# Performance work log

Hardware: AMD Instinct MI355X
Metric: run time of the kernel (lower is better)

## Reference

```python
import jax, jax.numpy as jnp
import numpy as np

L, D, H, B, SX, SY, VS, VT = 6, 1024, 16, 4, 512, 512, 32000, 32000
DK = D // H
FF = 4 * D
EPS = 1e-3          # LayerNorm eps (added to std, not var)
SCALE_EMB = float(np.sqrt(D))
NEG = -1e30         # stands in for -inf; fully-masked rows are zeroed after softmax


def pos_encoding(length, d):
    # tensor2tensor-style sinusoid: [sin | cos] concatenated along channels
    nt = d // 2
    lti = np.log(1e4) / (nt - 1)
    inv = np.exp(np.arange(nt) * -lti)
    st = np.arange(length)[:, None] * inv[None, :]
    return jnp.asarray(np.concatenate([np.sin(st), np.cos(st)], axis=1), jnp.float32)


def layer_norm(z, a, b):
    # faithful to the torch module: uses unbiased std (ddof=1) and divides by (std + eps)
    mu = z.mean(-1, keepdims=True)
    sig = jnp.sqrt(((z - mu) ** 2).sum(-1, keepdims=True) / (z.shape[-1] - 1))
    return (z - mu) / (sig + EPS) * a + b


def mha(xq, xkv, wq, wk, wv, wo, mask):
    # xq: (b, lq, D), xkv: (b, lk, D); head-chunking of channel dim == reshape to (H, DK)
    b, lq, _ = xq.shape
    q = (xq @ wq.T).reshape(b, lq, H, DK)
    k = (xkv @ wk.T).reshape(b, -1, H, DK)
    v = (xkv @ wv.T).reshape(b, -1, H, DK)
    s = jnp.einsum('bqhd,bkhd->bhqk', q, k) * (1.0 / np.sqrt(DK))
    m = mask[:, None, :, :]
    s = jnp.where(m, s, NEG)
    att = jax.nn.softmax(s, axis=-1)
    att = att * m.any(-1, keepdims=True)  # replicates NaN->0 for fully masked rows
    c = jnp.einsum('bhqk,bkhd->bqhd', att, v).reshape(b, lq, D)
    return c @ wo.T


def setup_inputs():
    key = jax.random.key(0)
    ks = jax.random.split(key, 10)
    s = 0.02
    emb_x = (jax.random.normal(ks[0], (VS, D), jnp.float32) * s).at[0].set(0.0)  # padding_idx=0
    emb_y = (jax.random.normal(ks[1], (VT, D), jnp.float32) * s).at[0].set(0.0)
    return {
        'emb_x': emb_x, 'emb_y': emb_y,
        'enc_qkvo': jax.random.normal(ks[2], (L, 4, D, D), jnp.float32) * s,
        'enc_ln_s': jnp.ones((L, 2, D), jnp.float32), 'enc_ln_b': jnp.zeros((L, 2, D), jnp.float32),
        'enc_w1': jax.random.normal(ks[3], (L, FF, D), jnp.float32) * s, 'enc_b1': jnp.zeros((L, FF), jnp.float32),
        'enc_w2': jax.random.normal(ks[4], (L, D, FF), jnp.float32) * s, 'enc_b2': jnp.zeros((L, D), jnp.float32),
        'dec_qkvo': jax.random.normal(ks[5], (L, 8, D, D), jnp.float32) * s,
        'dec_ln_s': jnp.ones((L, 3, D), jnp.float32), 'dec_ln_b': jnp.zeros((L, 3, D), jnp.float32),
        'dec_w1': jax.random.normal(ks[6], (L, FF, D), jnp.float32) * s, 'dec_b1': jnp.zeros((L, FF), jnp.float32),
        'dec_w2': jax.random.normal(ks[7], (L, D, FF), jnp.float32) * s, 'dec_b2': jnp.zeros((L, D), jnp.float32),
        'x_block': jax.random.randint(ks[8], (B, SX), 0, VS),
        'y_block': jax.random.randint(ks[9], (B, SY), 0, VT),
    }


def reference(emb_x, emb_y, enc_qkvo, enc_ln_s, enc_ln_b, enc_w1, enc_b1, enc_w2, enc_b2,
              dec_qkvo, dec_ln_s, dec_ln_b, dec_w1, dec_b1, dec_w2, dec_b2, x_block, y_block):
    # internal layout (b, len, D); torch code uses (b, D, len) -- math is identical
    ex = emb_x[x_block] * SCALE_EMB + pos_encoding(SX, D)[None]
    ey = emb_y[y_block] * SCALE_EMB + pos_encoding(SY, D)[None]
    xv = x_block != 0
    yv = y_block != 0
    xx = xv[:, :, None] & xv[:, None, :]                                   # (B, qx, kx)
    xy = yv[:, :, None] & xv[:, None, :]                                   # (B, qy, kx)
    yy = (yv[:, :, None] & yv[:, None, :]) & jnp.tril(jnp.ones((SY, SY), bool))[None]
    e = ex
    for i in range(L):
        sub = mha(e, e, enc_qkvo[i, 0], enc_qkvo[i, 1], enc_qkvo[i, 2], enc_qkvo[i, 3], xx)
        e = layer_norm(e + sub, enc_ln_s[i, 0], enc_ln_b[i, 0])
        sub = jax.nn.relu(e @ enc_w1[i].T + enc_b1[i]) @ enc_w2[i].T + enc_b2[i]
        e = layer_norm(e + sub, enc_ln_s[i, 1], enc_ln_b[i, 1])
    z = e
    e = ey
    for i in range(L):
        sub = mha(e, e, dec_qkvo[i, 0], dec_qkvo[i, 1], dec_qkvo[i, 2], dec_qkvo[i, 3], yy)
        e = layer_norm(e + sub, dec_ln_s[i, 0], dec_ln_b[i, 0])
        sub = mha(e, z, dec_qkvo[i, 4], dec_qkvo[i, 5], dec_qkvo[i, 6], dec_qkvo[i, 7], xy)
        e = layer_norm(e + sub, dec_ln_s[i, 1], dec_ln_b[i, 1])
        sub = jax.nn.relu(e @ dec_w1[i].T + dec_b1[i]) @ dec_w2[i].T + dec_b2[i]
        e = layer_norm(e + sub, dec_ln_s[i, 2], dec_ln_b[i, 2])
    return e @ emb_y.T  # tied output projection -> (B, SY, VT)
```

## Files before the change

kernel.cpp:

```cpp
#include <hip/hip_runtime.h>

typedef unsigned short u16;
typedef float f32x4 __attribute__((ext_vector_type(4)));
typedef __bf16 bf16x8 __attribute__((ext_vector_type(8)));
typedef u16 u16x8 __attribute__((ext_vector_type(8)));

#define DEV __device__ __forceinline__

DEV u16 f2bf(float f) {
  unsigned u = __builtin_bit_cast(unsigned, f);
  u += 0x7fffu + ((u >> 16) & 1u);
  return (u16)(u >> 16);
}

DEV float wsum(float v) {
#pragma unroll
  for (int o = 32; o > 0; o >>= 1) v += __shfl_xor(v, o, 64);
  return v;
}
DEV float gmax16(float v) {
#pragma unroll
  for (int o = 8; o > 0; o >>= 1) v = fmaxf(v, __shfl_xor(v, o, 64));
  return v;
}
DEV float gsum16(float v) {
#pragma unroll
  for (int o = 8; o > 0; o >>= 1) v += __shfl_xor(v, o, 64);
  return v;
}

DEV void gld16(const void* g, void* l) {
  __builtin_amdgcn_global_load_lds((const __attribute__((address_space(1))) void*)g,
                                   (__attribute__((address_space(3))) void*)l, 16, 0, 0);
}

template <int N>
DEV void vwait() {
  if constexpr (N == 0) asm volatile("s_waitcnt vmcnt(0)" ::: "memory");
  else if constexpr (N == 2) asm volatile("s_waitcnt vmcnt(2)" ::: "memory");
  else if constexpr (N == 4) asm volatile("s_waitcnt vmcnt(4)" ::: "memory");
  else asm volatile("s_waitcnt vmcnt(6)" ::: "memory");
}

DEV void remap_bxy(int& bx, int& by) {
  const int gx = gridDim.x, gy = gridDim.y;
  const int flat = blockIdx.y * gx + blockIdx.x;
  const int nwg = gx * gy;
  const int q = nwg >> 3, r = nwg & 7;
  const int xcd = flat & 7, li = flat >> 3;
  const int wg = (xcd < r ? xcd * (q + 1) : r * (q + 1) + (xcd - r) * q) + li;
  by = wg % gy;
  bx = wg / gy;
}

template <int BM, int BN, int MODE, int W>
__global__ __launch_bounds__(256, W) void gemm_k(
    const u16* __restrict__ A, const u16* __restrict__ B, int lda, int ldb, int K,
    float alpha, const float* __restrict__ bias, float* __restrict__ Cf, int ldc,
    u16* __restrict__ Cb, u16* __restrict__ qp, u16* __restrict__ kp,
    u16* __restrict__ vp, int n_off) {
  constexpr int FM = BM / 32, FN = BN / 32;
  constexpr int CHA = BM / 8, CHT = (BM + BN) / 8;
  __shared__ u16 lds[2][(BM + BN) * 64];
  const int lane = threadIdx.x & 63, wid = threadIdx.x >> 6;
  const int wr = wid >> 1, wc = wid & 1;
  int bx, by;
  remap_bxy(bx, by);
  const u16* gA = A + (long)(by * BM) * lda;
  const u16* gB = B + (long)(bx * BN) * ldb;

  const f32x4 zero4 = {0.f, 0.f, 0.f, 0.f};
  f32x4 acc[FM][FN];
#pragma unroll
  for (int m = 0; m < FM; ++m)
#pragma unroll
    for (int n = 0; n < FN; ++n) acc[m][n] = zero4;

  const int r8 = lane >> 3, sl = lane & 7;

  auto stage = [&](int buf, int kt) {
    const int kb = kt << 6;
#pragma unroll
    for (int c0 = 0; c0 < CHT; c0 += 4) {
      const int c = c0 + wid;
      u16* l = &lds[buf][c << 9];
      const u16* g;
      if (c < CHA) {
        int r = (c << 3) + r8;
        g = gA + (long)r * lda + kb + ((sl ^ (r & 7)) << 3);
      } else {
        int r = ((c - CHA) << 3) + r8;
        g = gB + (long)r * ldb + kb + ((sl ^ (r & 7)) << 3);
      }
      gld16(g, l);
    }
  };

  const int KT = K >> 6;
  stage(0, 0);
  __syncthreads();
  int cur = 0;
  for (int kt = 0; kt < KT; ++kt) {
    if (kt + 1 < KT) stage(cur ^ 1, kt + 1);
    const u16* lA = &lds[cur][0];
    const u16* lB = &lds[cur][BM << 6];
#pragma unroll
    for (int kk = 0; kk < 2; ++kk) {
      bf16x8 af[FM], bv[FN];
#pragma unroll
      for (int m = 0; m < FM; ++m) {
        int r = wr * (BM / 2) + m * 16 + (lane & 15);
        int slot = ((kk << 2) | (lane >> 4)) ^ (r & 7);
        af[m] = *(const bf16x8*)(lA + (r << 6) + (slot << 3));
      }
#pragma unroll
      for (int n = 0; n < FN; ++n) {
        int r = wc * (BN / 2) + n * 16 + (lane & 15);
        int slot = ((kk << 2) | (lane >> 4)) ^ (r & 7);
        bv[n] = *(const bf16x8*)(lB + (r << 6) + (slot << 3));
      }
#pragma unroll
      for (int m = 0; m < FM; ++m)
#pragma unroll
        for (int n = 0; n < FN; ++n)
          acc[m][n] = __builtin_amdgcn_mfma_f32_16x16x32_bf16(af[m], bv[n], acc[m][n], 0, 0, 0);
    }
    __syncthreads();
    cur ^= 1;
  }

  const int rb = by * BM + wr * (BM / 2) + ((lane >> 4) << 2);
  const int cb = bx * BN + wc * (BN / 2) + (lane & 15);
  if constexpr (MODE == 2) {
    const bool isV = (bx * BN + n_off) >= 2048;
    if (isV) {
      __syncthreads();
      u16* T = (u16*)&lds[0][0];
      constexpr int TS = BM + 8;
#pragma unroll
      for (int m = 0; m < FM; ++m)
#pragma unroll
        for (int n = 0; n < FN; ++n) {
          int cl = wc * (BN / 2) + n * 16 + (lane & 15);
#pragma unroll
          for (int j = 0; j < 4; ++j) {
            int rl = wr * (BM / 2) + m * 16 + ((lane >> 4) << 2) + j;
            T[cl * TS + rl] = f2bf(acc[m][n][j]);
          }
        }
      __syncthreads();
      const int vcb = bx * BN + n_off - 2048;
      const int b = (by * BM) >> 9, s0 = (by * BM) & 511;
#pragma unroll
      for (int p = 0; p < BM * BN / 2048; ++p) {
        int idx = p * 2048 + threadIdx.x * 8;
        int dl = idx / BM, slx = idx & (BM - 1);
        u16x8 o;
#pragma unroll
        for (int e = 0; e < 8; ++e) o[e] = T[dl * TS + slx + e];
        int vc = vcb + dl;
        *(u16x8*)(vp + (((long)b * 16 + (vc >> 6)) * 64 + (vc & 63)) * 512 + s0 + slx) = o;
      }
    } else {
#pragma unroll
      for (int m = 0; m < FM; ++m)
#pragma unroll
        for (int n = 0; n < FN; ++n)
#pragma unroll
          for (int j = 0; j < 4; ++j) {
            const int row = rb + m * 16 + j;
            const int np = cb + n * 16 + n_off;
            const int sel = np >> 10, dim = np & 1023;
            long base = (((long)(row >> 9) * 16 + (dim >> 6)) * 512 + (row & 511)) * 64 + (dim & 63);
            u16 val = f2bf(acc[m][n][j]);
            if (sel == 0) qp[base] = val;
            else kp[base] = val;
          }
    }
  } else {
#pragma unroll
    for (int m = 0; m < FM; ++m)
#pragma unroll
      for (int n = 0; n < FN; ++n)
#pragma unroll
        for (int j = 0; j < 4; ++j) {
          const int row = rb + m * 16 + j;
          const int col = cb + n * 16;
          float v = acc[m][n][j];
          if constexpr (MODE == 0) {
            float r = v * alpha;
            if (bias) r += bias[col];
            Cf[(long)row * ldc + col] = r;
          } else {
            Cb[(long)row * ldc + col] = f2bf(fmaxf(v + bias[col], 0.f));
          }
        }
  }
}

__global__ __launch_bounds__(512, 1) void gemm256_k(
    const u16* __restrict__ A, const u16* __restrict__ B, int lda, int ldb, int K,
    float* __restrict__ Cf, int ldc) {
  __shared__ u16 As[2][256 * 64];
  __shared__ u16 Bs[2][256 * 64];
  const int lane = threadIdx.x & 63, wid = threadIdx.x >> 6;
  const int wr = wid >> 2, wc = wid & 3;
  int bx, by;
  remap_bxy(bx, by);
  const u16* gA = A + (long)(by * 256) * lda;
  const u16* gB = B + (long)(bx * 256) * ldb;

  const f32x4 z4 = {0.f, 0.f, 0.f, 0.f};
  f32x4 acc[8][4];
#pragma unroll
  for (int m = 0; m < 8; ++m)
#pragma unroll
    for (int n = 0; n < 4; ++n) acc[m][n] = z4;

  const int ssl = lane & 7;

  auto stageH = [&](int t, int h) {
    const int kb = t << 6;
    const int buf = t & 1;
    const bool isA = (h == 0) || (h == 3);
    u16* ldsb = isA ? &As[buf][0] : &Bs[buf][0];
    const u16* gsrc = isA ? gA : gB;
    const int ld = isA ? lda : ldb;
    const int rbase = (h >= 2) ? 128 : 0;
#pragma unroll
    for (int rr = 0; rr < 2; ++rr) {
      const int r0 = rbase + rr * 64 + (wid << 3);
      const int r = r0 + (lane >> 3);
      gld16(gsrc + (long)r * ld + kb + ((ssl ^ (r & 7)) << 3), ldsb + (r0 << 6));
    }
  };

  const int KT = K >> 6;
  stageH(0, 0);
  stageH(0, 1);
  stageH(0, 2);
  stageH(0, 3);

  for (int t = 0; t < KT; ++t) {
    const int buf = t & 1;
    const bool more = (t + 1 < KT);
    const u16* lA = &As[buf][0];
    const u16* lB = &Bs[buf][0];
    bf16x8 af[4][2], bvl[2][2], bvh[2][2];

    vwait<4>();
    __builtin_amdgcn_s_barrier();
    __builtin_amdgcn_sched_barrier(0);
#pragma unroll
    for (int m = 0; m < 4; ++m)
#pragma unroll
      for (int kk = 0; kk < 2; ++kk) {
        int r = wr * 64 + m * 16 + (lane & 15);
        int sg = ((kk << 2) | (lane >> 4)) ^ (r & 7);
        af[m][kk] = *(const bf16x8*)(lA + (r << 6) + (sg << 3));
      }
#pragma unroll
    for (int n = 0; n < 2; ++n)
#pragma unroll
      for (int kk = 0; kk < 2; ++kk) {
        int c = wc * 32 + n * 16 + (lane & 15);
        int sg = ((kk << 2) | (lane >> 4)) ^ (c & 7);
        bvl[n][kk] = *(const bf16x8*)(lB + (c << 6) + (sg << 3));
      }
    if (more) stageH(t + 1, 0);
    __builtin_amdgcn_s_setprio(1);
#pragma unroll
    for (int kk = 0; kk < 2; ++kk)
#pragma unroll
      for (int m = 0; m < 4; ++m)
#pragma unroll
        for (int n = 0; n < 2; ++n)
          acc[m][n] = __builtin_amdgcn_mfma_f32_16x16x32_bf16(af[m][kk], bvl[n][kk], acc[m][n], 0, 0, 0);
    __builtin_amdgcn_s_setprio(0);

    if (more) vwait<4>();
    else vwait<2>();
    __builtin_amdgcn_s_barrier();
    __builtin_amdgcn_sched_barrier(0);
#pragma unroll
    for (int n = 0; n < 2; ++n)
#pragma unroll
      for (int kk = 0; kk < 2; ++kk) {
        int c = 128 + wc * 32 + n * 16 + (lane & 15);
        int sg = ((kk << 2) | (lane >> 4)) ^ (c & 7);
        bvh[n][kk] = *(const bf16x8*)(lB + (c << 6) + (sg << 3));
      }
    if (more) stageH(t + 1, 1);
    __builtin_amdgcn_s_setprio(1);
#pragma unroll
    for (int kk = 0; kk < 2; ++kk)
#pragma unroll
      for (int m = 0; m < 4; ++m)
#pragma unroll
        for (int n = 0; n < 2; ++n)
          acc[m][2 + n] = __builtin_amdgcn_mfma_f32_16x16x32_bf16(af[m][kk], bvh[n][kk], acc[m][2 + n], 0, 0, 0);
    __builtin_amdgcn_s_setprio(0);

    if (more) vwait<4>();
    else vwait<0>();
    __builtin_amdgcn_s_barrier();
    __builtin_amdgcn_sched_barrier(0);
#pragma unroll
    for (int m = 0; m < 4; ++m)
#pragma unroll
      for (int kk = 0; kk < 2; ++kk) {
        int r = 128 + wr * 64 + m * 16 + (lane & 15);
        int sg = ((kk << 2) | (lane >> 4)) ^ (r & 7);
        af[m][kk] = *(const bf16x8*)(lA + (r << 6) + (sg << 3));
      }
    if (more) stageH(t + 1, 2);
    __builtin_amdgcn_s_setprio(1);
#pragma unroll
    for (int kk = 0; kk < 2; ++kk)
#pragma unroll
      for (int m = 0; m < 4; ++m)
#pragma unroll
        for (int n = 0; n < 2; ++n)
          acc[4 + m][2 + n] = __builtin_amdgcn_mfma_f32_16x16x32_bf16(af[m][kk], bvh[n][kk], acc[4 + m][2 + n], 0, 0, 0);
    __builtin_amdgcn_s_setprio(0);

    __builtin_amdgcn_s_barrier();
    __builtin_amdgcn_sched_barrier(0);
    if (more) stageH(t + 1, 3);
    __builtin_amdgcn_s_setprio(1);
#pragma unroll
    for (int kk = 0; kk < 2; ++kk)
#pragma unroll
      for (int m = 0; m < 4; ++m)
#pragma unroll
        for (int n = 0; n < 2; ++n)
          acc[4 + m][n] = __builtin_amdgcn_mfma_f32_16x16x32_bf16(af[m][kk], bvl[n][kk], acc[4 + m][n], 0, 0, 0);
    __builtin_amdgcn_s_setprio(0);
  }

  const int rb = by * 256 + wr * 64 + ((lane >> 4) << 2);
  const int cb = bx * 256 + wc * 32 + (lane & 15);
#pragma unroll
  for (int mi = 0; mi < 8; ++mi)
#pragma unroll
    for (int ni = 0; ni < 4; ++ni)
#pragma unroll
      for (int j = 0; j < 4; ++j) {
        int row = rb + (mi & 3) * 16 + ((mi >> 2) << 7) + j;
        int col = cb + (ni & 1) * 16 + ((ni >> 1) << 7);
        Cf[(long)row * ldc + col] = acc[mi][ni][j];
      }
}

template <int CAUSAL>
__global__ __launch_bounds__(256, 2) void fattn_k(
    const u16* __restrict__ Qg, const u16* __restrict__ Kg, const u16* __restrict__ Vtg,
    const int* __restrict__ qids, const int* __restrict__ kids, u16* __restrict__ ctx) {
  __shared__ u16 Qs[128 * 64];
  __shared__ u16 Ks[2][64 * 64];
  __shared__ u16 Vs[2][64 * 64];
  __shared__ u16 Ps[4][32 * 64];
  const int lane = threadIdx.x & 63, wid = threadIdx.x >> 6;
  const int qt = blockIdx.x, bh = blockIdx.y, b = bh >> 4, h = bh & 15;
  const int q0 = qt << 7;
  const u16* Qbase = Qg + ((long)bh * 512 + q0) * 64;
  const u16* Kbase = Kg + (long)bh * 512 * 64;
  const u16* Vbase = Vtg + (long)bh * 64 * 512;
  const int r8 = lane >> 3, sl = lane & 7;

#pragma unroll
  for (int c0 = 0; c0 < 16; c0 += 4) {
    int c = c0 + wid;
    int r = (c << 3) + r8;
    gld16(Qbase + (long)r * 64 + ((sl ^ (r & 7)) << 3), &Qs[c << 9]);
  }

  auto stageKV = [&](int buf, int kt) {
#pragma unroll
    for (int c0 = 0; c0 < 16; c0 += 4) {
      int c = c0 + wid;
      if (c < 8) {
        int r = (c << 3) + r8;
        gld16(Kbase + (long)(kt * 64 + r) * 64 + ((sl ^ (r & 7)) << 3), &Ks[buf][c << 9]);
      } else {
        int r = ((c - 8) << 3) + r8;
        gld16(Vbase + (long)r * 512 + kt * 64 + ((sl ^ (r & 7)) << 3), &Vs[buf][(c - 8) << 9]);
      }
    }
  };

  const int NKT = CAUSAL ? ((q0 >> 6) + 2) : 8;
  stageKV(0, 0);
  __syncthreads();

  const f32x4 z4 = {0.f, 0.f, 0.f, 0.f};
  f32x4 oacc[2][4];
  float mrun[2][4], lrun[2][4];
  bool qv[2][4];
#pragma unroll
  for (int m = 0; m < 2; ++m)
#pragma unroll
    for (int j = 0; j < 4; ++j) {
      mrun[m][j] = -3e38f;
      lrun[m][j] = 0.f;
      int qg = q0 + wid * 32 + m * 16 + ((lane >> 4) << 2) + j;
      qv[m][j] = qids[(b << 9) + qg] != 0;
#pragma unroll
      for (int nd = 0; nd < 4; ++nd) oacc[m][nd] = z4;
    }

  int cur = 0;
  for (int kt = 0; kt < NKT; ++kt) {
    if (kt + 1 < NKT) stageKV(cur ^ 1, kt + 1);
    f32x4 s[2][4];
#pragma unroll
    for (int m = 0; m < 2; ++m)
#pragma unroll
      for (int n = 0; n < 4; ++n) s[m][n] = z4;
    __builtin_amdgcn_s_setprio(1);
#pragma unroll
    for (int kk = 0; kk < 2; ++kk) {
      bf16x8 aq[2], bk[4];
#pragma unroll
      for (int m = 0; m < 2; ++m) {
        int r = wid * 32 + m * 16 + (lane & 15);
        int slot = ((kk << 2) | (lane >> 4)) ^ (r & 7);
        aq[m] = *(const bf16x8*)&Qs[(r << 6) + (slot << 3)];
      }
#pragma unroll
      for (int n = 0; n < 4; ++n) {
        int c = n * 16 + (lane & 15);
        int slot = ((kk << 2) | (lane >> 4)) ^ (c & 7);
        bk[n] = *(const bf16x8*)&Ks[cur][(c << 6) + (slot << 3)];
      }
#pragma unroll
      for (int m = 0; m < 2; ++m)
#pragma unroll
        for (int n = 0; n < 4; ++n)
          s[m][n] = __builtin_amdgcn_mfma_f32_16x16x32_bf16(aq[m], bk[n], s[m][n], 0, 0, 0);
    }
    __builtin_amdgcn_s_setprio(0);
    bool kvld[4];
#pragma unroll
    for (int n = 0; n < 4; ++n)
      kvld[n] = kids[(b << 9) + (kt << 6) + (n << 4) + (lane & 15)] != 0;
    float mx[2][4];
#pragma unroll
    for (int m = 0; m < 2; ++m)
#pragma unroll
      for (int j = 0; j < 4; ++j) {
        mx[m][j] = -3e38f;
        int qg = q0 + wid * 32 + m * 16 + ((lane >> 4) << 2) + j;
#pragma unroll
        for (int n = 0; n < 4; ++n) {
          int colg = (kt << 6) + (n << 4) + (lane & 15);
          bool ok = qv[m][j] && kvld[n] && (!CAUSAL || colg <= qg);
          float sv = ok ? s[m][n][j] * 0.125f : -3e38f;
          s[m][n][j] = sv;
          mx[m][j] = fmaxf(mx[m][j], sv);
        }
        mx[m][j] = gmax16(mx[m][j]);
      }
#pragma unroll
    for (int m = 0; m < 2; ++m)
#pragma unroll
      for (int j = 0; j < 4; ++j) {
        float mn = fmaxf(mrun[m][j], mx[m][j]);
        float f = __expf(mrun[m][j] - mn);
        mrun[m][j] = mn;
        float ps = 0.f;
#pragma unroll
        for (int n = 0; n < 4; ++n) {
          float sv = s[m][n][j];
          float p = (sv > -1e37f) ? __expf(sv - mn) : 0.f;
          s[m][n][j] = p;
          ps += p;
        }
        ps = gsum16(ps);
        lrun[m][j] = lrun[m][j] * f + ps;
#pragma unroll
        for (int nd = 0; nd < 4; ++nd) oacc[m][nd][j] *= f;
      }
#pragma unroll
    for (int m = 0; m < 2; ++m)
#pragma unroll
      for (int n = 0; n < 4; ++n)
#pragma unroll
        for (int j = 0; j < 4; ++j) {
          int rl = (m << 4) + ((lane >> 4) << 2) + j;
          int slot = ((n << 1) | ((lane >> 3) & 1)) ^ (rl & 7);
          Ps[wid][(rl << 6) + (slot << 3) + (lane & 7)] = f2bf(s[m][n][j]);
        }
    __builtin_amdgcn_s_setprio(1);
#pragma unroll
    for (int kk = 0; kk < 2; ++kk) {
      bf16x8 pa[2], vv[4];
#pragma unroll
      for (int m = 0; m < 2; ++m) {
        int r = (m << 4) + (lane & 15);
        int slot = ((kk << 2) | (lane >> 4)) ^ (r & 7);
        pa[m] = *(const bf16x8*)&Ps[wid][(r << 6) + (slot << 3)];
      }
#pragma unroll
      for (int nd = 0; nd < 4; ++nd) {
        int rv = (nd << 4) + (lane & 15);
        int slot = ((kk << 2) | (lane >> 4)) ^ (rv & 7);
        vv[nd] = *(const bf16x8*)&Vs[cur][(rv << 6) + (slot << 3)];
      }
#pragma unroll
      for (int m = 0; m < 2; ++m)
#pragma unroll
        for (int nd = 0; nd < 4; ++nd)
          oacc[m][nd] = __builtin_amdgcn_mfma_f32_16x16x32_bf16(pa[m], vv[nd], oacc[m][nd], 0, 0, 0);
    }
    __builtin_amdgcn_s_setprio(0);
    __syncthreads();
    cur ^= 1;
  }
#pragma unroll
  for (int m = 0; m < 2; ++m)
#pragma unroll
    for (int j = 0; j < 4; ++j) {
      float inv = (lrun[m][j] > 0.f) ? 1.0f / lrun[m][j] : 0.f;
      int qg = q0 + wid * 32 + m * 16 + ((lane >> 4) << 2) + j;
      long rowb = (((long)(b << 9) + qg) * 16 + h) * 64;
#pragma unroll
      for (int nd = 0; nd < 4; ++nd) {
        int d = (nd << 4) + (lane & 15);
        ctx[rowb + d] = f2bf(oacc[m][nd][j] * inv);
      }
    }
}

__global__ __launch_bounds__(256) void embed_k(const int* __restrict__ ids,
                                               const float* __restrict__ emb,
                                               float* __restrict__ xo, u16* __restrict__ bfo) {
  const int tok = blockIdx.x, t = threadIdx.x;
  const int s = tok & 511;
  const long id = ids[tok];
  const int d = t * 4;
  float4 ev = *(const float4*)(emb + id * 1024 + d);
  float o[4] = {ev.x * 32.f, ev.y * 32.f, ev.z * 32.f, ev.w * 32.f};
#pragma unroll
  for (int j = 0; j < 4; ++j) {
    int dd = d + j, di = dd & 511;
    float ang = (float)s * expf(-(float)di * 0.0180241494559220821f);
    o[j] += (dd < 512) ? sinf(ang) : cosf(ang);
  }
  *(float4*)(xo + (long)tok * 1024 + d) = make_float4(o[0], o[1], o[2], o[3]);
  ushort4 ob = {f2bf(o[0]), f2bf(o[1]), f2bf(o[2]), f2bf(o[3])};
  *(ushort4*)(bfo + (long)tok * 1024 + d) = ob;
}

__global__ __launch_bounds__(256) void ln_k(const float* __restrict__ x,
                                            const float* __restrict__ sub,
                                            const float* __restrict__ gam,
                                            const float* __restrict__ bet,
                                            float* __restrict__ xo, u16* __restrict__ bfo) {
  __shared__ float red[8];
  const int row = blockIdx.x, t = threadIdx.x;
  const float4 xv = *(const float4*)(x + (long)row * 1024 + t * 4);
  const float4 sv = *(const float4*)(sub + (long)row * 1024 + t * 4);
  float v0 = xv.x + sv.x, v1 = xv.y + sv.y, v2 = xv.z + sv.z, v3 = xv.w + sv.w;
  float sm = wsum(v0 + v1 + v2 + v3);
  if ((t & 63) == 0) red[t >> 6] = sm;
  __syncthreads();
  const float mu = (red[0] + red[1] + red[2] + red[3]) * (1.0f / 1024.0f);
  const float d0 = v0 - mu, d1 = v1 - mu, d2 = v2 - mu, d3 = v3 - mu;
  float ss = wsum(d0 * d0 + d1 * d1 + d2 * d2 + d3 * d3);
  if ((t & 63) == 0) red[4 + (t >> 6)] = ss;
  __syncthreads();
  const float sig = sqrtf((red[4] + red[5] + red[6] + red[7]) * (1.0f / 1023.0f));
  const float inv = 1.0f / (sig + 0.001f);
  const float4 g4 = *(const float4*)(gam + t * 4);
  const float4 b4 = *(const float4*)(bet + t * 4);
  const float o0 = d0 * inv * g4.x + b4.x, o1 = d1 * inv * g4.y + b4.y;
  const float o2 = d2 * inv * g4.z + b4.z, o3 = d3 * inv * g4.w + b4.w;
  *(float4*)(xo + (long)row * 1024 + t * 4) = make_float4(o0, o1, o2, o3);
  ushort4 ob = {f2bf(o0), f2bf(o1), f2bf(o2), f2bf(o3)};
  *(ushort4*)(bfo + (long)row * 1024 + t * 4) = ob;
}

__global__ void cvt_k(const float* __restrict__ src, u16* __restrict__ dst, int n4) {
  for (int i = blockIdx.x * 256 + threadIdx.x; i < n4; i += gridDim.x * 256) {
    float4 v = ((const float4*)src)[i];
    ushort4 o = {f2bf(v.x), f2bf(v.y), f2bf(v.z), f2bf(v.w)};
    ((ushort4*)dst)[i] = o;
  }
}

__global__ void cvt3_k(const float* __restrict__ s0, int n0, const float* __restrict__ s1,
                       int n1, const float* __restrict__ s2, int n2, u16* __restrict__ dst) {
  const int tot = n0 + n1 + n2;
  for (int i = blockIdx.x * 256 + threadIdx.x; i < tot; i += gridDim.x * 256) {
    const float* s;
    int j;
    if (i < n0) { s = s0; j = i; }
    else if (i < n0 + n1) { s = s1; j = i - n0; }
    else { s = s2; j = i - n0 - n1; }
    float4 v = ((const float4*)s)[j];
    ushort4 o = {f2bf(v.x), f2bf(v.y), f2bf(v.z), f2bf(v.w)};
    ((ushort4*)dst)[i] = o;
  }
}

extern "C" void kernel_launch(void* const* d_in, const int* in_sizes, int n_in, void* d_out,
                              int out_size, void* d_ws, size_t ws_size, hipStream_t stream) {
  (void)in_sizes; (void)n_in; (void)out_size;
  const float* emb_x = (const float*)d_in[0];
  const float* emb_y = (const float*)d_in[1];
  const float* enc_qkvo = (const float*)d_in[2];
  const float* enc_ln_s = (const float*)d_in[3];
  const float* enc_ln_b = (const float*)d_in[4];
  const float* enc_w1 = (const float*)d_in[5];
  const float* enc_b1 = (const float*)d_in[6];
  const float* enc_w2 = (const float*)d_in[7];
  const float* enc_b2 = (const float*)d_in[8];
  const float* dec_qkvo = (const float*)d_in[9];
  const float* dec_ln_s = (const float*)d_in[10];
  const float* dec_ln_b = (const float*)d_in[11];
  const float* dec_w1 = (const float*)d_in[12];
  const float* dec_b1 = (const float*)d_in[13];
  const float* dec_w2 = (const float*)d_in[14];
  const float* dec_b2 = (const float*)d_in[15];
  const int* x_block = (const int*)d_in[16];
  const int* y_block = (const int*)d_in[17];

  const long TOK = 2048, Dm = 1024, M1 = 1048576;
  char* p = (char*)d_ws;
  auto alloc = [&](long bytes) { char* r = p; p += (bytes + 255) & ~255L; return r; };
  float* e32 = (float*)alloc(TOK * Dm * 4);
  float* sub = (float*)alloc(TOK * Dm * 4);
  u16* ebf = (u16*)alloc(TOK * Dm * 2);
  u16* zbf = (u16*)alloc(TOK * Dm * 2);
  u16* qb = (u16*)alloc(TOK * Dm * 2);
  u16* kb = (u16*)alloc(TOK * Dm * 2);
  u16* vtb = (u16*)alloc(TOK * Dm * 2);
  u16* ctx = (u16*)alloc(TOK * Dm * 2);
  u16* hbuf = (u16*)alloc(TOK * 4096 * 2);
  u16* wbuf = (u16*)alloc(16L * M1 * 2);
  u16* embyb = (u16*)alloc(32000L * 1024 * 2);
  if ((size_t)(p - (char*)d_ws) > ws_size) return;

  auto gemmF = [&](const u16* A, const u16* Bw, int M, int N, int K, int lda, int ldb,
                   float alpha, const float* bias, float* C, int ldc) {
    dim3 g(N / 64, M / 64);
    gemm_k<64, 64, 0, 4><<<g, 256, 0, stream>>>(A, Bw, lda, ldb, K, alpha, bias, C, ldc,
                                                nullptr, nullptr, nullptr, nullptr, 0);
  };
  auto gemmRelu = [&](const u16* A, const u16* Bw, const float* bias, u16* C) {
    dim3 g(32, 16);
    gemm_k<128, 128, 1, 2><<<g, 256, 0, stream>>>(A, Bw, 1024, 1024, 1024, 1.f, bias, nullptr,
                                                  4096, C, nullptr, nullptr, nullptr, 0);
  };
  auto gemmQKV = [&](const u16* A, const u16* Bw, int N, int n_off) {
    if (N >= 2048) {
      dim3 g(N / 128, 32);
      gemm_k<64, 128, 2, 3><<<g, 256, 0, stream>>>(A, Bw, 1024, 1024, 1024, 1.f, nullptr,
                                                   nullptr, 0, nullptr, qb, kb, vtb, n_off);
    } else {
      dim3 g(N / 64, 32);
      gemm_k<64, 64, 2, 4><<<g, 256, 0, stream>>>(A, Bw, 1024, 1024, 1024, 1.f, nullptr,
                                                  nullptr, 0, nullptr, qb, kb, vtb, n_off);
    }
  };
  auto attn = [&](const int* qids, const int* kids, int causal) {
    if (causal)
      fattn_k<1><<<dim3(4, 64), 256, 0, stream>>>(qb, kb, vtb, qids, kids, ctx);
    else
      fattn_k<0><<<dim3(4, 64), 256, 0, stream>>>(qb, kb, vtb, qids, kids, ctx);
  };
  auto lnorm = [&](const float* g, const float* b) {
    ln_k<<<2048, 256, 0, stream>>>(e32, sub, g, b, e32, ebf);
  };

  cvt_k<<<2048, 256, 0, stream>>>(emb_y, embyb, 32000 * 1024 / 4);

  embed_k<<<2048, 256, 0, stream>>>(x_block, emb_x, e32, ebf);
  for (int i = 0; i < 6; ++i) {
    cvt3_k<<<2048, 256, 0, stream>>>(enc_qkvo + (long)i * 4 * M1, (int)M1,
                                     enc_w1 + (long)i * 4 * M1, (int)M1,
                                     enc_w2 + (long)i * 4 * M1, (int)M1, wbuf);
    gemmQKV(ebf, wbuf, 3072, 0);
    attn(x_block, x_block, 0);
    gemmF(ctx, wbuf + 3L * M1, 2048, 1024, 1024, 1024, 1024, 1.f, nullptr, sub, 1024);
    lnorm(enc_ln_s + (i * 2 + 0) * 1024, enc_ln_b + (i * 2 + 0) * 1024);
    gemmRelu(ebf, wbuf + 4L * M1, enc_b1 + i * 4096, hbuf);
    gemmF(hbuf, wbuf + 8L * M1, 2048, 1024, 4096, 4096, 4096, 1.f, enc_b2 + i * 1024, sub, 1024);
    lnorm(enc_ln_s + (i * 2 + 1) * 1024, enc_ln_b + (i * 2 + 1) * 1024);
  }
  hipMemcpyAsync(zbf, ebf, TOK * Dm * 2, hipMemcpyDeviceToDevice, stream);

  embed_k<<<2048, 256, 0, stream>>>(y_block, emb_y, e32, ebf);
  for (int i = 0; i < 6; ++i) {
    cvt3_k<<<2048, 256, 0, stream>>>(dec_qkvo + (long)i * 8 * M1, (int)(2 * M1),
                                     dec_w1 + (long)i * 4 * M1, (int)M1,
                                     dec_w2 + (long)i * 4 * M1, (int)M1, wbuf);
    gemmQKV(ebf, wbuf, 3072, 0);
    attn(y_block, y_block, 1);
    gemmF(ctx, wbuf + 3L * M1, 2048, 1024, 1024, 1024, 1024, 1.f, nullptr, sub, 1024);
    lnorm(dec_ln_s + (i * 3 + 0) * 1024, dec_ln_b + (i * 3 + 0) * 1024);
    gemmQKV(ebf, wbuf + 4L * M1, 1024, 0);
    gemmQKV(zbf, wbuf + 5L * M1, 2048, 1024);
    attn(y_block, x_block, 0);
    gemmF(ctx, wbuf + 7L * M1, 2048, 1024, 1024, 1024, 1024, 1.f, nullptr, sub, 1024);
    lnorm(dec_ln_s + (i * 3 + 1) * 1024, dec_ln_b + (i * 3 + 1) * 1024);
    gemmRelu(ebf, wbuf + 8L * M1, dec_b1 + i * 4096, hbuf);
    gemmF(hbuf, wbuf + 12L * M1, 2048, 1024, 4096, 4096, 4096, 1.f, dec_b2 + i * 1024, sub, 1024);
    lnorm(dec_ln_s + (i * 3 + 2) * 1024, dec_ln_b + (i * 3 + 2) * 1024);
  }
  gemm256_k<<<dim3(125, 8), 512, 0, stream>>>(ebf, embyb, 1024, 1024, 1024,
                                              (float*)d_out, 32000);
}
```

Measured before the change: 2.410 ms.

## Fuse residual add into GEMM epilogue, deepen K tile, widen attention blocks

The residual add moves from the layernorm kernel into the fp32 GEMM epilogue, so layernorm reads one tensor instead of two. The fp32 output GEMMs now stage 128-wide K tiles with lower occupancy, halving the barrier count per K loop. The attention kernel goes from 4 to 8 waves per block, each wave handling 16 query rows instead of 32, which reduces per-wave registers and adds parallelism. The larger LDS footprint and lower occupancy hint in the GEMM may offset some of the gains.

Result: faster. 2.276 ms (-5.6%).

```diff
diff --git a/kernel.cpp b/kernel.cpp
--- a/kernel.cpp
+++ b/kernel.cpp
@@ -53,15 +53,16 @@
   bx = wg / gy;
 }
 
-template <int BM, int BN, int MODE, int W>
+template <int BM, int BN, int MODE, int W, int BK>
 __global__ __launch_bounds__(256, W) void gemm_k(
     const u16* __restrict__ A, const u16* __restrict__ B, int lda, int ldb, int K,
-    float alpha, const float* __restrict__ bias, float* __restrict__ Cf, int ldc,
-    u16* __restrict__ Cb, u16* __restrict__ qp, u16* __restrict__ kp,
-    u16* __restrict__ vp, int n_off) {
+    float alpha, const float* __restrict__ bias, const float* __restrict__ resid,
+    float* __restrict__ Cf, int ldc, u16* __restrict__ Cb, u16* __restrict__ qp,
+    u16* __restrict__ kp, u16* __restrict__ vp, int n_off) {
   constexpr int FM = BM / 32, FN = BN / 32;
   constexpr int CHA = BM / 8, CHT = (BM + BN) / 8;
-  __shared__ u16 lds[2][(BM + BN) * 64];
+  constexpr int KCH = BK / 64;
+  __shared__ u16 lds[2][(BM + BN) * BK];
   const int lane = threadIdx.x & 63, wid = threadIdx.x >> 6;
   const int wr = wid >> 1, wc = wid & 1;
   int bx, by;
@@ -79,44 +80,49 @@
   const int r8 = lane >> 3, sl = lane & 7;
 
   auto stage = [&](int buf, int kt) {
-    const int kb = kt << 6;
-#pragma unroll
-    for (int c0 = 0; c0 < CHT; c0 += 4) {
-      const int c = c0 + wid;
-      u16* l = &lds[buf][c << 9];
-      const u16* g;
-      if (c < CHA) {
-        int r = (c << 3) + r8;
-        g = gA + (long)r * lda + kb + ((sl ^ (r & 7)) << 3);
-      } else {
-        int r = ((c - CHA) << 3) + r8;
-        g = gB + (long)r * ldb + kb + ((sl ^ (r & 7)) << 3);
-      }
-      gld16(g, l);
+#pragma unroll
+    for (int sub = 0; sub < KCH; ++sub) {
+      const int kb = kt * BK + (sub << 6);
+      u16* lbase = &lds[buf][sub * (BM + BN) * 64];
+#pragma unroll
+      for (int c0 = 0; c0 < CHT; c0 += 4) {
+        const int c = c0 + wid;
+        u16* l = lbase + (c << 9);
+        const u16* g;
+        if (c < CHA) {
+          int r = (c << 3) + r8;
+          g = gA + (long)r * lda + kb + ((sl ^ (r & 7)) << 3);
+        } else {
+          int r = ((c - CHA) << 3) + r8;
+          g = gB + (long)r * ldb + kb + ((sl ^ (r & 7)) << 3);
+        }
+        gld16(g, l);
+      }
     }
   };
 
-  const int KT = K >> 6;
+  const int KT = K / BK;
   stage(0, 0);
   __syncthreads();
   int cur = 0;
   for (int kt = 0; kt < KT; ++kt) {
     if (kt + 1 < KT) stage(cur ^ 1, kt + 1);
-    const u16* lA = &lds[cur][0];
-    const u16* lB = &lds[cur][BM << 6];
-#pragma unroll
-    for (int kk = 0; kk < 2; ++kk) {
+#pragma unroll
+    for (int q = 0; q < 2 * KCH; ++q) {
+      const int kh = q >> 1, kl = q & 1;
+      const u16* lA = &lds[cur][kh * (BM + BN) * 64];
+      const u16* lB = lA + (BM << 6);
       bf16x8 af[FM], bv[FN];
 #pragma unroll
       for (int m = 0; m < FM; ++m) {
         int r = wr * (BM / 2) + m * 16 + (lane & 15);
-        int slot = ((kk << 2) | (lane >> 4)) ^ (r & 7);
+        int slot = ((kl << 2) | (lane >> 4)) ^ (r & 7);
         af[m] = *(const bf16x8*)(lA + (r << 6) + (slot << 3));
       }
 #pragma unroll
       for (int n = 0; n < FN; ++n) {
         int r = wc * (BN / 2) + n * 16 + (lane & 15);
-        int slot = ((kk << 2) | (lane >> 4)) ^ (r & 7);
+        int slot = ((kl << 2) | (lane >> 4)) ^ (r & 7);
         bv[n] = *(const bf16x8*)(lB + (r << 6) + (slot << 3));
       }
 #pragma unroll
@@ -190,6 +196,7 @@
           if constexpr (MODE == 0) {
             float r = v * alpha;
             if (bias) r += bias[col];
+            if (resid) r += resid[(long)row * ldc + col];
             Cf[(long)row * ldc + col] = r;
           } else {
             Cb[(long)row * ldc + col] = f2bf(fmaxf(v + bias[col], 0.f));
@@ -353,13 +360,13 @@
 }
 
 template <int CAUSAL>
-__global__ __launch_bounds__(256, 2) void fattn_k(
+__global__ __launch_bounds__(512, 2) void fattn_k(
     const u16* __restrict__ Qg, const u16* __restrict__ Kg, const u16* __restrict__ Vtg,
     const int* __restrict__ qids, const int* __restrict__ kids, u16* __restrict__ ctx) {
   __shared__ u16 Qs[128 * 64];
   __shared__ u16 Ks[2][64 * 64];
   __shared__ u16 Vs[2][64 * 64];
-  __shared__ u16 Ps[4][32 * 64];
+  __shared__ u16 Ps[8][16 * 64];
   const int lane = threadIdx.x & 63, wid = threadIdx.x >> 6;
   const int qt = blockIdx.x, bh = blockIdx.y, b = bh >> 4, h = bh & 15;
   const int q0 = qt << 7;
@@ -369,7 +376,7 @@
   const int r8 = lane >> 3, sl = lane & 7;
 
 #pragma unroll
-  for (int c0 = 0; c0 < 16; c0 += 4) {
+  for (int c0 = 0; c0 < 16; c0 += 8) {
     int c = c0 + wid;
     int r = (c << 3) + r8;
     gld16(Qbase + (long)r * 64 + ((sl ^ (r & 7)) << 3), &Qs[c << 9]);
@@ -377,7 +384,7 @@
 
   auto stageKV = [&](int buf, int kt) {
 #pragma unroll
-    for (int c0 = 0; c0 < 16; c0 += 4) {
+    for (int c0 = 0; c0 < 16; c0 += 8) {
       int c = c0 + wid;
       if (c < 8) {
         int r = (c << 3) + r8;
@@ -394,142 +401,120 @@
   __syncthreads();
 
   const f32x4 z4 = {0.f, 0.f, 0.f, 0.f};
-  f32x4 oacc[2][4];
-  float mrun[2][4], lrun[2][4];
-  bool qv[2][4];
-#pragma unroll
-  for (int m = 0; m < 2; ++m)
-#pragma unroll
-    for (int j = 0; j < 4; ++j) {
-      mrun[m][j] = -3e38f;
-      lrun[m][j] = 0.f;
-      int qg = q0 + wid * 32 + m * 16 + ((lane >> 4) << 2) + j;
-      qv[m][j] = qids[(b << 9) + qg] != 0;
-#pragma unroll
-      for (int nd = 0; nd < 4; ++nd) oacc[m][nd] = z4;
-    }
+  f32x4 oacc[4];
+  float mrun[4], lrun[4];
+  bool qv[4];
+#pragma unroll
+  for (int j = 0; j < 4; ++j) {
+    mrun[j] = -3e38f;
+    lrun[j] = 0.f;
+    int qg = q0 + wid * 16 + ((lane >> 4) << 2) + j;
+    qv[j] = qids[(b << 9) + qg] != 0;
+  }
+#pragma unroll
+  for (int nd = 0; nd < 4; ++nd) oacc[nd] = z4;
 
   int cur = 0;
   for (int kt = 0; kt < NKT; ++kt) {
     if (kt + 1 < NKT) stageKV(cur ^ 1, kt + 1);
-    f32x4 s[2][4];
-#pragma unroll
-    for (int m = 0; m < 2; ++m)
-#pragma unroll
-      for (int n = 0; n < 4; ++n) s[m][n] = z4;
+    f32x4 s[4];
+#pragma unroll
+    for (int n = 0; n < 4; ++n) s[n] = z4;
     __builtin_amdgcn_s_setprio(1);
 #pragma unroll
     for (int kk = 0; kk < 2; ++kk) {
-      bf16x8 aq[2], bk[4];
-#pragma unroll
-      for (int m = 0; m < 2; ++m) {
-        int r = wid * 32 + m * 16 + (lane & 15);
-        int slot = ((kk << 2) | (lane >> 4)) ^ (r & 7);
-        aq[m] = *(const bf16x8*)&Qs[(r << 6) + (slot << 3)];
-      }
+      bf16x8 aq, bk[4];
+      int r = wid * 16 + (lane & 15);
+      int slot = ((kk << 2) | (lane >> 4)) ^ (r & 7);
+      aq = *(const bf16x8*)&Qs[(r << 6) + (slot << 3)];
 #pragma unroll
       for (int n = 0; n < 4; ++n) {
         int c = n * 16 + (lane & 15);
-        int slot = ((kk << 2) | (lane >> 4)) ^ (c & 7);
-        bk[n] = *(const bf16x8*)&Ks[cur][(c << 6) + (slot << 3)];
-      }
-#pragma unroll
-      for (int m = 0; m < 2; ++m)
-#pragma unroll
-        for (int n = 0; n < 4; ++n)
-          s[m][n] = __builtin_amdgcn_mfma_f32_16x16x32_bf16(aq[m], bk[n], s[m][n], 0, 0, 0);
+        int slt = ((kk << 2) | (lane >> 4)) ^ (c & 7);
+        bk[n] = *(const bf16x8*)&Ks[cur][(c << 6) + (slt << 3)];
+      }
+#pragma unroll
+      for (int n = 0; n < 4; ++n)
+        s[n] = __builtin_amdgcn_mfma_f32_16x16x32_bf16(aq, bk[n], s[n], 0, 0, 0);
     }
     __builtin_amdgcn_s_setprio(0);
     bool kvld[4];
 #pragma unroll
     for (int n = 0; n < 4; ++n)
       kvld[n] = kids[(b << 9) + (kt << 6) + (n << 4) + (lane & 15)] != 0;
-    float mx[2][4];
-#pragma unroll
-    for (int m = 0; m < 2; ++m)
+    float mx[4];
+#pragma unroll
+    for (int j = 0; j < 4; ++j) {
+      mx[j] = -3e38f;
+      int qg = q0 + wid * 16 + ((lane >> 4) << 2) + j;
+#pragma unroll
+      for (int n = 0; n < 4; ++n) {
+        int colg = (kt << 6) + (n << 4) + (lane & 15);
+        bool ok = qv[j] && kvld[n] && (!CAUSAL || colg <= qg);
+        float sv = ok ? s[n][j] * 0.125f : -3e38f;
+        s[n][j] = sv;
+        mx[j] = fmaxf(mx[j], sv);
+      }
+      mx[j] = gmax16(mx[j]);
+    }
+#pragma unroll
+    for (int j = 0; j < 4; ++j) {
+      float mn = fmaxf(mrun[j], mx[j]);
+      float f = __expf(mrun[j] - mn);
+      mrun[j] = mn;
+      float ps = 0.f;
+#pragma unroll
+      for (int n = 0; n < 4; ++n) {
+        float sv = s[n][j];
+        float p = (sv > -1e37f) ? __expf(sv - mn) : 0.f;
+        s[n][j] = p;
+        ps += p;
+      }
+      ps = gsum16(ps);
+      lrun[j] = lrun[j] * f + ps;
+#pragma unroll
+      for (int nd = 0; nd < 4; ++nd) oacc[nd][j] *= f;
+    }
+#pragma unroll
+    for (int n = 0; n < 4; ++n)
 #pragma unroll
       for (int j = 0; j < 4; ++j) {
-        mx[m][j] = -3e38f;
-        int qg = q0 + wid * 32 + m * 16 + ((lane >> 4) << 2) + j;
-#pragma unroll
-        for (int n = 0; n < 4; ++n) {
-          int colg = (kt << 6) + (n << 4) + (lane & 15);
-          bool ok = qv[m][j] && kvld[n] && (!CAUSAL || colg <= qg);
-          float sv = ok ? s[m][n][j] * 0.125f : -3e38f;
-          s[m][n][j] = sv;
-          mx[m][j] = fmaxf(mx[m][j], sv);
-        }
-        mx[m][j] = gmax16(mx[m][j]);
-      }
-#pragma unroll
-    for (int m = 0; m < 2; ++m)
-#pragma unroll
-      for (int j = 0; j < 4; ++j) {
-        float mn = fmaxf(mrun[m][j], mx[m][j]);
-        float f = __expf(mrun[m][j] - mn);
-        mrun[m][j] = mn;
-        float ps = 0.f;
-#pragma unroll
-        for (int n = 0; n < 4; ++n) {
-          float sv = s[m][n][j];
-          float p = (sv > -1e37f) ? __expf(sv - mn) : 0.f;
-          s[m][n][j] = p;
-          ps += p;
-        }
-        ps = gsum16(ps);
-        lrun[m][j] = lrun[m][j] * f + ps;
-#pragma unroll
-        for (int nd = 0; nd < 4; ++nd) oacc[m][nd][j] *= f;
-      }
-#pragma unroll
-    for (int m = 0; m < 2; ++m)
-#pragma unroll
-      for (int n = 0; n < 4; ++n)
-#pragma unroll
-        for (int j = 0; j < 4; ++j) {
-          int rl = (m << 4) + ((lane >> 4) << 2) + j;
-          int slot = ((n << 1) | ((lane >> 3) & 1)) ^ (rl & 7);
-          Ps[wid][(rl << 6) + (slot << 3) + (lane & 7)] = f2bf(s[m][n][j]);
-        }
+        int rl = ((lane >> 4) << 2) + j;
+        int slot = ((n << 1) | ((lane >> 3) & 1)) ^ (rl & 7);
+        Ps[wid][(rl << 6) + (slot << 3) + (lane & 7)] = f2bf(s[n][j]);
+      }
     __builtin_amdgcn_s_setprio(1);
 #pragma unroll
     for (int kk = 0; kk < 2; ++kk) {
-      bf16x8 pa[2], vv[4];
-#pragma unroll
-      for (int m = 0; m < 2; ++m) {
-        int r = (m << 4) + (lane & 15);
-        int slot = ((kk << 2) | (lane >> 4)) ^ (r & 7);
-        pa[m] = *(const bf16x8*)&Ps[wid][(r << 6) + (slot << 3)];
-      }
+      bf16x8 pa, vv[4];
+      int r = lane & 15;
+      int slot = ((kk << 2) | (lane >> 4)) ^ (r & 7);
+      pa = *(const bf16x8*)&Ps[wid][(r << 6) + (slot << 3)];
 #pragma unroll
       for (int nd = 0; nd < 4; ++nd) {
         int rv = (nd << 4) + (lane & 15);
-        int slot = ((kk << 2) | (lane >> 4)) ^ (rv & 7);
-        vv[nd] = *(const bf16x8*)&Vs[cur][(rv << 6) + (slot << 3)];
-      }
-#pragma unroll
-      for (int m = 0; m < 2; ++m)
-#pragma unroll
-        for (int nd = 0; nd < 4; ++nd)
-          oacc[m][nd] = __builtin_amdgcn_mfma_f32_16x16x32_bf16(pa[m], vv[nd], oacc[m][nd], 0, 0, 0);
+        int slt = ((kk << 2) | (lane >> 4)) ^ (rv & 7);
+        vv[nd] = *(const bf16x8*)&Vs[cur][(rv << 6) + (slt << 3)];
+      }
+#pragma unroll
+      for (int nd = 0; nd < 4; ++nd)
+        oacc[nd] = __builtin_amdgcn_mfma_f32_16x16x32_bf16(pa, vv[nd], oacc[nd], 0, 0, 0);
     }
     __builtin_amdgcn_s_setprio(0);
     __syncthreads();
     cur ^= 1;
   }
 #pragma unroll
-  for (int m = 0; m < 2; ++m)
-#pragma unroll
-    for (int j = 0; j < 4; ++j) {
-      float inv = (lrun[m][j] > 0.f) ? 1.0f / lrun[m][j] : 0.f;
-      int qg = q0 + wid * 32 + m * 16 + ((lane >> 4) << 2) + j;
-      long rowb = (((long)(b << 9) + qg) * 16 + h) * 64;
-#pragma unroll
-      for (int nd = 0; nd < 4; ++nd) {
-        int d = (nd << 4) + (lane & 15);
-        ctx[rowb + d] = f2bf(oacc[m][nd][j] * inv);
-      }
-    }
+  for (int j = 0; j < 4; ++j) {
+    float inv = (lrun[j] > 0.f) ? 1.0f / lrun[j] : 0.f;
+    int qg = q0 + wid * 16 + ((lane >> 4) << 2) + j;
+    long rowb = (((long)(b << 9) + qg) * 16 + h) * 64;
+#pragma unroll
+    for (int nd = 0; nd < 4; ++nd) {
+      int d = (nd << 4) + (lane & 15);
+      ctx[rowb + d] = f2bf(oacc[nd][j] * inv);
+    }
+  }
 }
 
 __global__ __launch_bounds__(256) void embed_k(const int* __restrict__ ids,
@@ -552,16 +537,14 @@
   *(ushort4*)(bfo + (long)tok * 1024 + d) = ob;
 }
 
-__global__ __launch_bounds__(256) void ln_k(const float* __restrict__ x,
-                                            const float* __restrict__ sub,
+__global__ __launch_bounds__(256) void ln_k(const float* __restrict__ vin,
                                             const float* __restrict__ gam,
                                             const float* __restrict__ bet,
                                             float* __restrict__ xo, u16* __restrict__ bfo) {
   __shared__ float red[8];
   const int row = blockIdx.x, t = threadIdx.x;
-  const float4 xv = *(const float4*)(x + (long)row * 1024 + t * 4);
-  const float4 sv = *(const float4*)(sub + (long)row * 1024 + t * 4);
-  float v0 = xv.x + sv.x, v1 = xv.y + sv.y, v2 = xv.z + sv.z, v3 = xv.w + sv.w;
+  const float4 xv = *(const float4*)(vin + (long)row * 1024 + t * 4);
+  float v0 = xv.x, v1 = xv.y, v2 = xv.z, v3 = xv.w;
   float sm = wsum(v0 + v1 + v2 + v3);
   if ((t & 63) == 0) red[t >> 6] = sm;
   __syncthreads();
@@ -643,35 +626,39 @@
   if ((size_t)(p - (char*)d_ws) > ws_size) return;
 
   auto gemmF = [&](const u16* A, const u16* Bw, int M, int N, int K, int lda, int ldb,
-                   float alpha, const float* bias, float* C, int ldc) {
+                   float alpha, const float* bias, const float* resid, float* C, int ldc) {
     dim3 g(N / 64, M / 64);
-    gemm_k<64, 64, 0, 4><<<g, 256, 0, stream>>>(A, Bw, lda, ldb, K, alpha, bias, C, ldc,
-                                                nullptr, nullptr, nullptr, nullptr, 0);
+    gemm_k<64, 64, 0, 2, 128><<<g, 256, 0, stream>>>(A, Bw, lda, ldb, K, alpha, bias, resid,
+                                                     C, ldc, nullptr, nullptr, nullptr,
+                                                     nullptr, 0);
   };
   auto gemmRelu = [&](const u16* A, const u16* Bw, const float* bias, u16* C) {
     dim3 g(32, 16);
-    gemm_k<128, 128, 1, 2><<<g, 256, 0, stream>>>(A, Bw, 1024, 1024, 1024, 1.f, bias, nullptr,
-                                                  4096, C, nullptr, nullptr, nullptr, 0);
+    gemm_k<128, 128, 1, 2, 64><<<g, 256, 0, stream>>>(A, Bw, 1024, 1024, 1024, 1.f, bias,
+                                                      nullptr, nullptr, 4096, C, nullptr,
+                                                      nullptr, nullptr, 0);
   };
   auto gemmQKV = [&](const u16* A, const u16* Bw, int N, int n_off) {
     if (N >= 2048) {
       dim3 g(N / 128, 32);
-      gemm_k<64, 128, 2, 3><<<g, 256, 0, stream>>>(A, Bw, 1024, 1024, 1024, 1.f, nullptr,
-                                                   nullptr, 0, nullptr, qb, kb, vtb, n_off);
+      gemm_k<64, 128, 2, 3, 64><<<g, 256, 0, stream>>>(A, Bw, 1024, 1024, 1024, 1.f, nullptr,
+                                                       nullptr, nullptr, 0, nullptr, qb, kb,
+                                                       vtb, n_off);
     } else {
       dim3 g(N / 64, 32);
-      gemm_k<64, 64, 2, 4><<<g, 256, 0, stream>>>(A, Bw, 1024, 1024, 1024, 1.f, nullptr,
-                                                  nullptr, 0, nullptr, qb, kb, vtb, n_off);
+      gemm_k<64, 64, 2, 4, 64><<<g, 256, 0, stream>>>(A, Bw, 1024, 1024, 1024, 1.f, nullptr,
+                                                      nullptr, nullptr, 0, nullptr, qb, kb,
+                                                      vtb, n_off);
     }
   };
   auto attn = [&](const int* qids, const int* kids, int causal) {
     if (causal)
-      fattn_k<1><<<dim3(4, 64), 256, 0, stream>>>(qb, kb, vtb, qids, kids, ctx);
+      fattn_k<1><<<dim3(4, 64), 512, 0, stream>>>(qb, kb, vtb, qids, kids, ctx);
     else
-      fattn_k<0><<<dim3(4, 64), 256, 0, stream>>>(qb, kb, vtb, qids, kids, ctx);
+      fattn_k<0><<<dim3(4, 64), 512, 0, stream>>>(qb, kb, vtb, qids, kids, ctx);
   };
   auto lnorm = [&](const float* g, const float* b) {
-    ln_k<<<2048, 256, 0, stream>>>(e32, sub, g, b, e32, ebf);
+    ln_k<<<2048, 256, 0, stream>>>(sub, g, b, e32, ebf);
   };
 
   cvt_k<<<2048, 256, 0, stream>>>(emb_y, embyb, 32000 * 1024 / 4);
@@ -683,10 +670,11 @@
                                      enc_w2 + (long)i * 4 * M1, (int)M1, wbuf);
     gemmQKV(ebf, wbuf, 3072, 0);
     attn(x_block, x_block, 0);
-    gemmF(ctx, wbuf + 3L * M1, 2048, 1024, 1024, 1024, 1024, 1.f, nullptr, sub, 1024);
+    gemmF(ctx, wbuf + 3L * M1, 2048, 1024, 1024, 1024, 1024, 1.f, nullptr, e32, sub, 1024);
     lnorm(enc_ln_s + (i * 2 + 0) * 1024, enc_ln_b + (i * 2 + 0) * 1024);
     gemmRelu(ebf, wbuf + 4L * M1, enc_b1 + i * 4096, hbuf);
-    gemmF(hbuf, wbuf + 8L * M1, 2048, 1024, 4096, 4096, 4096, 1.f, enc_b2 + i * 1024, sub, 1024);
+    gemmF(hbuf, wbuf + 8L * M1, 2048, 1024, 4096, 4096, 4096, 1.f, enc_b2 + i * 1024, e32,
+          sub, 1024);
     lnorm(enc_ln_s + (i * 2 + 1) * 1024, enc_ln_b + (i * 2 + 1) * 1024);
   }
   hipMemcpyAsync(zbf, ebf, TOK * Dm * 2, hipMemcpyDeviceToDevice, stream);
@@ -698,15 +686,16 @@
                                      dec_w2 + (long)i * 4 * M1, (int)M1, wbuf);
     gemmQKV(ebf, wbuf, 3072, 0);
     attn(y_block, y_block, 1);
-    gemmF(ctx, wbuf + 3L * M1, 2048, 1024, 1024, 1024, 1024, 1.f, nullptr, sub, 1024);
+    gemmF(ctx, wbuf + 3L * M1, 2048, 1024, 1024, 1024, 1024, 1.f, nullptr, e32, sub, 1024);
     lnorm(dec_ln_s + (i * 3 + 0) * 1024, dec_ln_b + (i * 3 + 0) * 1024);
     gemmQKV(ebf, wbuf + 4L * M1, 1024, 0);
     gemmQKV(zbf, wbuf + 5L * M1, 2048, 1024);
     attn(y_block, x_block, 0);
-    gemmF(ctx, wbuf + 7L * M1, 2048, 1024, 1024, 1024, 1024, 1.f, nullptr, sub, 1024);
+    gemmF(ctx, wbuf + 7L * M1, 2048, 1024, 1024, 1024, 1024, 1.f, nullptr, e32, sub, 1024);
     lnorm(dec_ln_s + (i * 3 + 1) * 1024, dec_ln_b + (i * 3 + 1) * 1024);
     gemmRelu(ebf, wbuf + 8L * M1, dec_b1 + i * 4096, hbuf);
-    gemmF(hbuf, wbuf + 12L * M1, 2048, 1024, 4096, 4096, 4096, 1.f, dec_b2 + i * 1024, sub, 1024);
+    gemmF(hbuf, wbuf + 12L * M1, 2048, 1024, 4096, 4096, 4096, 1.f, dec_b2 + i * 1024, e32,
+          sub, 1024);
     lnorm(dec_ln_s + (i * 3 + 2) * 1024, dec_ln_b + (i * 3 + 2) * 1024);
   }
   gemm256_k<<<dim3(125, 8), 512, 0, stream>>>(ebf, embyb, 1024, 1024, 1024,
```
